# Optimization experiments

Hardware: AMD Instinct MI355X
Metric: run time of the kernel (lower is better)

The kernel has to match this reference:

```python
import jax, jax.numpy as jnp
import numpy as np

EPS = 1e-5

def _ln(x):
    # non-affine LayerNorm over last dim
    m = jnp.mean(x, axis=-1, keepdims=True)
    v = jnp.var(x, axis=-1, keepdims=True)
    return (x - m) / jnp.sqrt(v + EPS)

def setup_inputs() -> dict:
    key = jax.random.key(0)
    ks = jax.random.split(key, 6)
    B, D_in, H = 16384, 512, 512
    bound_i = 1.0 / np.sqrt(D_in)
    bound_h = 1.0 / np.sqrt(H)
    x = jax.random.normal(ks[0], (B, D_in), dtype=jnp.float32)
    hx = jax.random.normal(ks[1], (B, H), dtype=jnp.float32)
    W_i2h = jax.random.uniform(ks[2], (3 * H, D_in), minval=-bound_i, maxval=bound_i, dtype=jnp.float32)
    b_i2h = jax.random.uniform(ks[3], (3 * H,), minval=-bound_i, maxval=bound_i, dtype=jnp.float32)
    W_h2h = jax.random.uniform(ks[4], (3 * H, H), minval=-bound_h, maxval=bound_h, dtype=jnp.float32)
    b_h2h = jax.random.uniform(ks[5], (3 * H,), minval=-bound_h, maxval=bound_h, dtype=jnp.float32)
    return {"x": x, "hx": hx, "W_i2h": W_i2h, "b_i2h": b_i2h, "W_h2h": W_h2h, "b_h2h": b_h2h}

def reference(x, hx, W_i2h, b_i2h, W_h2h, b_h2h):
    H = hx.shape[-1]
    xt = x @ W_i2h.T + b_i2h        # [B, 3H]
    ht = hx @ W_h2h.T + b_h2h       # [B, 3H]
    x_new = xt[:, 2 * H:]
    h_new = ht[:, 2 * H:]
    gates = jax.nn.sigmoid(_ln(xt[:, : 2 * H]) + _ln(ht[:, : 2 * H]))
    r_t = gates[:, :H]
    z_t = gates[:, H:]
    n_t = jnp.tanh(_ln(x_new) + r_t * _ln(h_new))
    h_t = z_t * hx + (1.0 - z_t) * n_t
    return h_t
```

## Files before the change

### kernel.cpp

```cpp
#include <hip/hip_runtime.h>

#define M_ROWS 16384
#define N_COLS 1536
#define K_DIM  512
#define H_DIM  512
#define NT     8

typedef __attribute__((ext_vector_type(8))) short short8;
typedef __attribute__((ext_vector_type(16))) float f32x16;

__device__ __forceinline__ unsigned short f2bf(float f) {
  unsigned u = __float_as_uint(f);
  u += 0x7fffu + ((u >> 16) & 1u);
  return (unsigned short)(u >> 16);
}
__device__ __forceinline__ float bf2f(unsigned short h) {
  return __uint_as_float(((unsigned)h) << 16);
}
__device__ __forceinline__ unsigned cvt_pk_bf16(float lo, float hi) {
  unsigned r;
  asm("v_cvt_pk_bf16_f32 %0, %1, %2" : "=v"(r) : "v"(lo), "v"(hi));
  return r;
}

__device__ __forceinline__ void gload_lds16(const void* g, void* l) {
  __builtin_amdgcn_global_load_lds((const __attribute__((address_space(1))) void*)g,
                                   (__attribute__((address_space(3))) void*)l,
                                   16, 0, 0);
}

__global__ __launch_bounds__(256) void cvt_w(
    const float* __restrict__ Wi, const float* __restrict__ Wh,
    unsigned short* __restrict__ Wib, unsigned short* __restrict__ Whb) {
  int i = blockIdx.x * blockDim.x + threadIdx.x;
  const float* s; unsigned short* d; int off;
  if (i < 196608) { s = Wi; d = Wib; off = i; }
  else            { s = Wh; d = Whb; off = i - 196608; }
  float4 f = ((const float4*)s)[off];
  ushort4 u;
  u.x = f2bf(f.x); u.y = f2bf(f.y); u.z = f2bf(f.z); u.w = f2bf(f.w);
  ((ushort4*)d)[off] = u;
}

__global__ __launch_bounds__(256, 3) void gemm_bf16(
    const float* __restrict__ x, const float* __restrict__ hx,
    const unsigned short* __restrict__ Wib, const unsigned short* __restrict__ Whb,
    const float* __restrict__ b_i2h, const float* __restrict__ b_h2h,
    unsigned short* __restrict__ xt, unsigned short* __restrict__ ht) {
  const int mat = blockIdx.z;
  const float* A32         = mat ? hx : x;
  const unsigned short* Bw = mat ? Whb : Wib;
  const float* bias        = mat ? b_h2h : b_i2h;
  unsigned short* outp     = mat ? ht : xt;

  const int m0 = blockIdx.x * 128;
  const int n0 = blockIdx.y * 128;

  __shared__ short lds[3 * 128 * 64];
  short* ldsA = lds;
  short* ldsB = lds + 128 * 64;

  const int t = threadIdx.x;
  const int w = t >> 6, lane = t & 63;
  const int w_row = w >> 1, w_col = w & 1;
  const int l31 = lane & 31, h = lane >> 5;
  const int srow = lane >> 3;
  const int scol = ((lane & 7) ^ srow) * 8;

  const int arow_s = w * 32 + (lane >> 3);
  const int ag = lane & 7;
  float4 areg[8];
  auto issueA = [&](int kt) {
    const int k0 = kt * 64;
#pragma unroll
    for (int s = 0; s < 4; ++s) {
      const float* src = A32 + (size_t)(m0 + arow_s + s * 8) * K_DIM + k0 + ag * 8;
      areg[2 * s]     = *(const float4*)src;
      areg[2 * s + 1] = *(const float4*)(src + 4);
    }
  };
  auto issueB = [&](int kt) {
    short* sB = ldsB + (kt & 1) * 8192;
    const int k0 = kt * 64;
#pragma unroll
    for (int q = 0; q < 4; ++q) {
      const int br = w * 32 + q * 8;
      gload_lds16(Bw + (size_t)(n0 + br + srow) * K_DIM + k0 + scol, &sB[br * 64]);
    }
  };
  auto writeA = [&]() {
#pragma unroll
    for (int s = 0; s < 4; ++s) {
      const int r = arow_s + s * 8;
      float4 f0 = areg[2 * s], f1 = areg[2 * s + 1];
      uint4 u;
      u.x = cvt_pk_bf16(f0.x, f0.y);
      u.y = cvt_pk_bf16(f0.z, f0.w);
      u.z = cvt_pk_bf16(f1.x, f1.y);
      u.w = cvt_pk_bf16(f1.z, f1.w);
      *(uint4*)&ldsA[r * 64 + ((ag ^ (r & 7)) * 8)] = u;
    }
  };

  f32x16 acc[2][2];
#pragma unroll
  for (int i = 0; i < 2; ++i)
#pragma unroll
    for (int j = 0; j < 2; ++j)
#pragma unroll
      for (int r = 0; r < 16; ++r) acc[i][j][r] = 0.f;

  issueA(0);
  issueB(0);

  for (int kt = 0; kt < NT; ++kt) {
    writeA();
    __syncthreads();
    if (kt < NT - 1) {
      issueA(kt + 1);
      issueB(kt + 1);
    }
    const short* lB = ldsB + (kt & 1) * 8192;
#pragma unroll
    for (int kk = 0; kk < 4; ++kk) {
      const int chunk = ((kk * 2 + h) ^ (l31 & 7)) * 8;
      short8 af[2], bfr[2];
#pragma unroll
      for (int i = 0; i < 2; ++i)
        af[i] = *(const short8*)&ldsA[(w_row * 64 + i * 32 + l31) * 64 + chunk];
#pragma unroll
      for (int j = 0; j < 2; ++j)
        bfr[j] = *(const short8*)&lB[(w_col * 64 + j * 32 + l31) * 64 + chunk];
      __builtin_amdgcn_s_setprio(1);
#pragma unroll
      for (int i = 0; i < 2; ++i)
#pragma unroll
        for (int j = 0; j < 2; ++j)
          acc[i][j] = __builtin_amdgcn_mfma_f32_32x32x16_bf16(af[i], bfr[j], acc[i][j], 0, 0, 0);
      __builtin_amdgcn_s_setprio(0);
    }
    if (kt < NT - 1) {
      asm volatile("" ::: "memory");
      __builtin_amdgcn_s_barrier();
      asm volatile("" ::: "memory");
    }
  }

  const float biasj0 = bias[n0 + w_col * 64 + l31];
  const float biasj1 = bias[n0 + w_col * 64 + 32 + l31];
#pragma unroll
  for (int i = 0; i < 2; ++i) {
#pragma unroll
    for (int g = 0; g < 4; ++g) {
#pragma unroll
      for (int d = 0; d < 4; ++d) {
        const int reg = g * 4 + d;
        const int row = d + 8 * g + 4 * h;
        ushort2 pk;
        pk.x = f2bf(acc[i][0][reg] + biasj0);
        pk.y = f2bf(acc[i][1][reg] + biasj1);
        *(ushort2*)(outp + (size_t)(m0 + w_row * 64 + i * 32 + row) * N_COLS +
                    n0 + w_col * 64 + 2 * l31) = pk;
      }
    }
  }
}

__global__ __launch_bounds__(256) void finalize_kernel(
    const unsigned short* __restrict__ xt, const unsigned short* __restrict__ ht,
    const float* __restrict__ hx, float* __restrict__ out) {
  const int w = threadIdx.x >> 6, lane = threadIdx.x & 63;
  const int b = blockIdx.x * 4 + w;
  const size_t rb = (size_t)b * N_COLS;

  short8 sxr = *(const short8*)&xt[rb + 8 * lane];
  short8 sxz = *(const short8*)&xt[rb + 512 + 8 * lane];
  short8 sxn = *(const short8*)&xt[rb + 1024 + 8 * lane];
  short8 shr = *(const short8*)&ht[rb + 8 * lane];
  short8 shz = *(const short8*)&ht[rb + 512 + 8 * lane];
  short8 shn = *(const short8*)&ht[rb + 1024 + 8 * lane];

  float vxr[8], vxz[8], vxn[8], vhr[8], vhz[8], vhn[8];
#pragma unroll
  for (int k = 0; k < 8; ++k) {
    vxr[k] = bf2f((unsigned short)sxr[k]);
    vxz[k] = bf2f((unsigned short)sxz[k]);
    vxn[k] = bf2f((unsigned short)sxn[k]);
    vhr[k] = bf2f((unsigned short)shr[k]);
    vhz[k] = bf2f((unsigned short)shz[k]);
    vhn[k] = bf2f((unsigned short)shn[k]);
  }

  float pr[8] = {0.f, 0.f, 0.f, 0.f, 0.f, 0.f, 0.f, 0.f};
#pragma unroll
  for (int k = 0; k < 8; ++k) {
    pr[0] += vxr[k] + vxz[k];
    pr[1] += vxr[k] * vxr[k] + vxz[k] * vxz[k];
    pr[2] += vxn[k];
    pr[3] += vxn[k] * vxn[k];
    pr[4] += vhr[k] + vhz[k];
    pr[5] += vhr[k] * vhr[k] + vhz[k] * vhz[k];
    pr[6] += vhn[k];
    pr[7] += vhn[k] * vhn[k];
  }
#pragma unroll
  for (int msk = 1; msk < 64; msk <<= 1)
#pragma unroll
    for (int k = 0; k < 8; ++k) pr[k] += __shfl_xor(pr[k], msk);

  const float inv2H = 1.f / 1024.f, invH = 1.f / 512.f;
  const float mx0 = pr[0] * inv2H;
  const float ix0 = rsqrtf(pr[1] * inv2H - mx0 * mx0 + 1e-5f);
  const float mx1 = pr[2] * invH;
  const float ix1 = rsqrtf(pr[3] * invH - mx1 * mx1 + 1e-5f);
  const float mh0 = pr[4] * inv2H;
  const float ih0 = rsqrtf(pr[5] * inv2H - mh0 * mh0 + 1e-5f);
  const float mh1 = pr[6] * invH;
  const float ih1 = rsqrtf(pr[7] * invH - mh1 * mh1 + 1e-5f);

  auto calc = [&](float xrv, float xzv, float xnv, float hrv, float hzv,
                  float hnv, float hxs) -> float {
    float ar = (xrv - mx0) * ix0 + (hrv - mh0) * ih0;
    float az = (xzv - mx0) * ix0 + (hzv - mh0) * ih0;
    float r = 1.f / (1.f + __expf(-ar));
    float z = 1.f / (1.f + __expf(-az));
    float arg = (xnv - mx1) * ix1 + r * ((hnv - mh1) * ih1);
    float e2 = __expf(2.f * arg);
    float nn = (e2 - 1.f) / (e2 + 1.f);
    return z * hxs + (1.f - z) * nn;
  };

  const int base4 = 64 * (lane >> 3) + 4 * (lane & 7);
  const float* hxrow = hx + (size_t)b * H_DIM;
  float* orow = out + (size_t)b * H_DIM;

  float4 hx0 = *(const float4*)&hxrow[base4];
  float4 hx1 = *(const float4*)&hxrow[base4 + 32];
  const float* h0p = (const float*)&hx0;
  const float* h1p = (const float*)&hx1;

  float4 r0, r1;
  float* r0p = (float*)&r0;
  float* r1p = (float*)&r1;
#pragma unroll
  for (int k = 0; k < 4; ++k) {
    r0p[k] = calc(vxr[2 * k], vxz[2 * k], vxn[2 * k],
                  vhr[2 * k], vhz[2 * k], vhn[2 * k], h0p[k]);
    r1p[k] = calc(vxr[2 * k + 1], vxz[2 * k + 1], vxn[2 * k + 1],
                  vhr[2 * k + 1], vhz[2 * k + 1], vhn[2 * k + 1], h1p[k]);
  }
  *(float4*)&orow[base4] = r0;
  *(float4*)&orow[base4 + 32] = r1;
}

extern "C" void kernel_launch(void* const* d_in, const int* in_sizes, int n_in,
                              void* d_out, int out_size, void* d_ws, size_t ws_size,
                              hipStream_t stream) {
  const float* x  = (const float*)d_in[0];
  const float* hx = (const float*)d_in[1];
  const float* Wi = (const float*)d_in[2];
  const float* bi = (const float*)d_in[3];
  const float* Wh = (const float*)d_in[4];
  const float* bh = (const float*)d_in[5];
  float* out = (float*)d_out;

  char* ws = (char*)d_ws;
  unsigned short* Wib = (unsigned short*)(ws);
  unsigned short* Whb = (unsigned short*)(ws + 1572864);
  unsigned short* xt  = (unsigned short*)(ws + 3145728);
  unsigned short* ht  = (unsigned short*)(ws + 53477376);

  cvt_w<<<1536, 256, 0, stream>>>(Wi, Wh, Wib, Whb);

  gemm_bf16<<<dim3(M_ROWS / 128, N_COLS / 128, 2), 256, 0, stream>>>(
      x, hx, Wib, Whb, bi, bh, xt, ht);

  finalize_kernel<<<M_ROWS / 4, 256, 0, stream>>>(xt, ht, hx, out);
}
```

Measured before the change: 205.9 us.

## Stage fp32 A tiles directly into LDS and convert to bf16 at fragment load

The GEMM kernel now copies the fp32 activation tile straight into shared memory with global-to-LDS loads, using a new XOR swizzle. Each wave converts to bf16 when it reads its MFMA fragments, replacing the earlier path that loaded into registers, converted, then wrote LDS. The double-buffered B tile and the prefetch of the next k-step are dropped in favour of a simple load, sync, compute, sync loop, and the setprio hints are removed. This frees registers and removes the VGPR staging and LDS write step. The cost is no overlap between loads and MFMA, twice the LDS traffic for A, and conversion work that is repeated across waves sharing the same rows.

```diff
diff --git a/kernel.cpp b/kernel.cpp
--- a/kernel.cpp
+++ b/kernel.cpp
@@ -56,9 +56,8 @@
   const int m0 = blockIdx.x * 128;
   const int n0 = blockIdx.y * 128;
 
-  __shared__ short lds[3 * 128 * 64];
-  short* ldsA = lds;
-  short* ldsB = lds + 128 * 64;
+  __shared__ float ldsA[128 * 64];
+  __shared__ short ldsB[128 * 64];
 
   const int t = threadIdx.x;
   const int w = t >> 6, lane = t & 63;
@@ -66,84 +65,61 @@
   const int l31 = lane & 31, h = lane >> 5;
   const int srow = lane >> 3;
   const int scol = ((lane & 7) ^ srow) * 8;
-
-  const int arow_s = w * 32 + (lane >> 3);
-  const int ag = lane & 7;
-  float4 areg[8];
-  auto issueA = [&](int kt) {
+  const int swA = ((l31 & 7) << 1) ^ ((l31 >> 3) & 1);
+
+  f32x16 acc[2][2];
+#pragma unroll
+  for (int i = 0; i < 2; ++i)
+#pragma unroll
+    for (int j = 0; j < 2; ++j)
+#pragma unroll
+      for (int r = 0; r < 16; ++r) acc[i][j][r] = 0.f;
+
+  for (int kt = 0; kt < NT; ++kt) {
     const int k0 = kt * 64;
 #pragma unroll
-    for (int s = 0; s < 4; ++s) {
-      const float* src = A32 + (size_t)(m0 + arow_s + s * 8) * K_DIM + k0 + ag * 8;
-      areg[2 * s]     = *(const float4*)src;
-      areg[2 * s + 1] = *(const float4*)(src + 4);
-    }
-  };
-  auto issueB = [&](int kt) {
-    short* sB = ldsB + (kt & 1) * 8192;
-    const int k0 = kt * 64;
-#pragma unroll
-    for (int q = 0; q < 4; ++q) {
-      const int br = w * 32 + q * 8;
-      gload_lds16(Bw + (size_t)(n0 + br + srow) * K_DIM + k0 + scol, &sB[br * 64]);
-    }
-  };
-  auto writeA = [&]() {
-#pragma unroll
-    for (int s = 0; s < 4; ++s) {
-      const int r = arow_s + s * 8;
-      float4 f0 = areg[2 * s], f1 = areg[2 * s + 1];
-      uint4 u;
-      u.x = cvt_pk_bf16(f0.x, f0.y);
-      u.y = cvt_pk_bf16(f0.z, f0.w);
-      u.z = cvt_pk_bf16(f1.x, f1.y);
-      u.w = cvt_pk_bf16(f1.z, f1.w);
-      *(uint4*)&ldsA[r * 64 + ((ag ^ (r & 7)) * 8)] = u;
-    }
-  };
-
-  f32x16 acc[2][2];
-#pragma unroll
-  for (int i = 0; i < 2; ++i)
-#pragma unroll
-    for (int j = 0; j < 2; ++j)
-#pragma unroll
-      for (int r = 0; r < 16; ++r) acc[i][j][r] = 0.f;
-
-  issueA(0);
-  issueB(0);
-
-  for (int kt = 0; kt < NT; ++kt) {
-    writeA();
+    for (int q = 0; q < 8; ++q) {
+      const int R = w * 32 + q * 4;
+      const int r = R + (lane >> 4);
+      const int j = (lane & 15) ^ ((r & 7) << 1) ^ ((r >> 3) & 1);
+      gload_lds16(A32 + (size_t)(m0 + r) * K_DIM + k0 + j * 4, &ldsA[R * 64]);
+    }
+#pragma unroll
+    for (int q2 = 0; q2 < 4; ++q2) {
+      const int br = w * 32 + q2 * 8;
+      gload_lds16(Bw + (size_t)(n0 + br + srow) * K_DIM + k0 + scol, &ldsB[br * 64]);
+    }
     __syncthreads();
-    if (kt < NT - 1) {
-      issueA(kt + 1);
-      issueB(kt + 1);
-    }
-    const short* lB = ldsB + (kt & 1) * 8192;
+
 #pragma unroll
     for (int kk = 0; kk < 4; ++kk) {
+      const int j0 = kk * 4 + 2 * h;
+      const int p0 = (j0 ^ swA) * 4;
+      const int p1 = ((j0 + 1) ^ swA) * 4;
+      short8 af[2], bfr[2];
+#pragma unroll
+      for (int i = 0; i < 2; ++i) {
+        const float* rowp = &ldsA[(w_row * 64 + i * 32 + l31) * 64];
+        float4 fa0 = *(const float4*)&rowp[p0];
+        float4 fa1 = *(const float4*)&rowp[p1];
+        union { uint4 u; short8 s; } cv;
+        cv.u.x = cvt_pk_bf16(fa0.x, fa0.y);
+        cv.u.y = cvt_pk_bf16(fa0.z, fa0.w);
+        cv.u.z = cvt_pk_bf16(fa1.x, fa1.y);
+        cv.u.w = cvt_pk_bf16(fa1.z, fa1.w);
+        af[i] = cv.s;
+      }
       const int chunk = ((kk * 2 + h) ^ (l31 & 7)) * 8;
-      short8 af[2], bfr[2];
-#pragma unroll
-      for (int i = 0; i < 2; ++i)
-        af[i] = *(const short8*)&ldsA[(w_row * 64 + i * 32 + l31) * 64 + chunk];
 #pragma unroll
       for (int j = 0; j < 2; ++j)
-        bfr[j] = *(const short8*)&lB[(w_col * 64 + j * 32 + l31) * 64 + chunk];
-      __builtin_amdgcn_s_setprio(1);
+        bfr[j] = *(const short8*)&ldsB[(w_col * 64 + j * 32 + l31) * 64 + chunk];
 #pragma unroll
       for (int i = 0; i < 2; ++i)
 #pragma unroll
         for (int j = 0; j < 2; ++j)
           acc[i][j] = __builtin_amdgcn_mfma_f32_32x32x16_bf16(af[i], bfr[j], acc[i][j], 0, 0, 0);
-      __builtin_amdgcn_s_setprio(0);
-    }
-    if (kt < NT - 1) {
-      asm volatile("" ::: "memory");
-      __builtin_amdgcn_s_barrier();
-      asm volatile("" ::: "memory");
-    }
+    }
+    __syncthreads();
   }
 
   const float biasj0 = bias[n0 + w_col * 64 + l31];
```

Measured after the change: 205.1 us. No clear change (-0.4%).
